# Kernel tuning notes

Measured on AMD Instinct MI355X. Metric: run time of the kernel, lower is better.

The kernel has to match this reference:

```python
import jax, jax.numpy as jnp
import numpy as np

B, C_IN, C_OUT, T, N, KS = 16, 64, 64, 48, 1024, 3

def setup_inputs() -> dict:
    key = jax.random.key(0)
    k1, k2, k3, k4 = jax.random.split(key, 4)
    x = jax.random.normal(k1, (B, C_IN, T, N), dtype=jnp.float32)
    Lk = jax.random.normal(k2, (KS, N, N), dtype=jnp.float32) / np.sqrt(N)
    # kaiming-uniform-like init for theta, uniform for b
    fan_in = C_IN * KS
    bound_t = np.sqrt(6.0 / fan_in)
    theta = jax.random.uniform(k3, (C_IN, C_OUT, KS), dtype=jnp.float32,
                               minval=-bound_t, maxval=bound_t)
    bound_b = 1.0 / np.sqrt(fan_in)
    b = jax.random.uniform(k4, (1, C_OUT, 1, 1), dtype=jnp.float32,
                           minval=-bound_b, maxval=bound_b)
    return {"x": x, "Lk": Lk, "theta": theta, "b": b}

def reference(x, Lk, theta, b):
    # x: [B, c_in, T, N], Lk: [ks, N, N], theta: [c_in, c_out, ks], b: [1, c_out, 1, 1]
    x_c = jnp.einsum('knm,bitm->bitkn', Lk, x)          # [B, c_in, T, ks, N]
    x_gc = jnp.einsum('iok,bitkn->botn', theta, x_c) + b  # [B, c_out, T, N]
    # Align: c_in == c_out -> identity
    return jax.nn.relu(x_gc + x)
```

## Files before the change

kernel.cpp:

```cpp
#include <hip/hip_runtime.h>
#include <hip/hip_bf16.h>
#include <stdint.h>


typedef short bs8 __attribute__((ext_vector_type(8)));
typedef float f32x4 __attribute__((ext_vector_type(4)));

#define NB   16
#define NC   64
#define NT   48
#define NN   1024
#define NKS  3
#define KDIM 3072
#define KT   48

__device__ __forceinline__ short f2bs(float f) {
  uint32_t u = __builtin_bit_cast(uint32_t, f);
  u = (u + 0x7FFFu + ((u >> 16) & 1u)) >> 16;
  return (short)u;
}

__device__ __forceinline__ void gload16(const void* g, void* l) {
  __builtin_amdgcn_global_load_lds(
      (const __attribute__((address_space(1))) void*)g,
      (__attribute__((address_space(3))) void*)l, 16, 0, 0);
}

__global__ __launch_bounds__(256) void k_prep_bt(const float* __restrict__ Lk,
                                                 short* __restrict__ BT) {
  int gid = blockIdx.x * 256 + threadIdx.x;
  int e = gid * 4;
  int k = e >> 20;
  int rem = e & 1048575;
  int n = rem >> 10;
  int m = rem & 1023;
  float4 v = *reinterpret_cast<const float4*>(Lk + e);
  union { short s[4]; uint64_t u; } p;
  p.s[0] = f2bs(v.x); p.s[1] = f2bs(v.y); p.s[2] = f2bs(v.z); p.s[3] = f2bs(v.w);
  *reinterpret_cast<uint64_t*>(BT + (size_t)n * KDIM + k * NN + m) = p.u;
}

__global__ __launch_bounds__(256, 2) void k_step1(const float* __restrict__ x,
                                                  const float* __restrict__ theta,
                                                  short* __restrict__ Y, int b0) {
  __shared__ __align__(16) short th[NKS * 64 * 72];
  __shared__ __align__(16) float xs[64 * 128];
  int tid = threadIdx.x;
  int wave = tid >> 6;
  for (int idx = tid; idx < NC * NC * NKS; idx += 256) {
    int i = idx / (NC * NKS);
    int r = idx - i * (NC * NKS);
    int o = r / NKS;
    int k = r - o * NKS;
    th[(k * 64 + o) * 72 + i] = f2bs(theta[idx]);
  }

  int bid = blockIdx.x;
  int mt  = bid & 7;
  int btl = bid >> 3;
  int b_l = btl / NT;
  int t   = btl - b_l * NT;
  int b   = b0 + b_l;
  const float* xb = x + (size_t)b * (NC * NT * NN) + (size_t)t * NN + mt * 128;

#pragma unroll
  for (int c = 0; c < 8; ++c) {
    int idx = c * 256 + tid;
    int row = idx >> 5, ch = idx & 31;
    gload16(xb + (size_t)row * (NT * NN) + ch * 4,
            xs + (c * 256 + wave * 64) * 4);
  }
  __syncthreads();

  int lane = tid & 63;
  int l15 = lane & 15, lg = lane >> 4;
  size_t yrow0 = (size_t)btl * 64;

  for (int nni = 0; nni < 2; ++nni) {
    int mloc = wave * 32 + nni * 16 + l15;
    float xv[16];
#pragma unroll
    for (int j = 0; j < 16; ++j) {
      int i = ((j >> 3) << 5) + lg * 8 + (j & 7);
      xv[j] = xs[i * 128 + mloc];
    }
    f32x4 acc[3][4];
#pragma unroll
    for (int k = 0; k < 3; ++k)
#pragma unroll
      for (int mi = 0; mi < 4; ++mi)
        acc[k][mi] = (f32x4){0.f, 0.f, 0.f, 0.f};

#pragma unroll
    for (int ks = 0; ks < 2; ++ks) {
      bs8 bfrag;
#pragma unroll
      for (int j = 0; j < 8; ++j) bfrag[j] = f2bs(xv[ks * 8 + j]);
#pragma unroll
      for (int mi = 0; mi < 4; ++mi) {
#pragma unroll
        for (int k = 0; k < 3; ++k) {
          const bs8* ap = reinterpret_cast<const bs8*>(
              &th[(k * 64 + mi * 16 + l15) * 72 + ks * 32 + lg * 8]);
          acc[k][mi] = __builtin_amdgcn_mfma_f32_16x16x32_bf16(
              *ap, bfrag, acc[k][mi], 0, 0, 0);
        }
      }
    }
    int mcol = mt * 128 + mloc;
#pragma unroll
    for (int k = 0; k < 3; ++k)
#pragma unroll
      for (int mi = 0; mi < 4; ++mi)
#pragma unroll
        for (int q = 0; q < 4; ++q) {
          int o = mi * 16 + lg * 4 + q;
          Y[(yrow0 + o) * KDIM + k * NN + mcol] = f2bs(acc[k][mi][q]);
        }
  }
}


__device__ __forceinline__ void stage_tile(const short* __restrict__ src,
                                           short* lds, int tid) {
  int wave = tid >> 6;
#pragma unroll
  for (int c = 0; c < 4; ++c) {
    int idx = c * 256 + tid;
    int row = idx >> 3, c8 = idx & 7;
    int c8s = c8 ^ (row & 7);
    gload16(src + (size_t)row * KDIM + c8s * 8,
            lds + (c * 256 + wave * 64) * 8);
  }
}

#define VMC(N) asm volatile("s_waitcnt vmcnt(" #N ")" ::: "memory")
#define BARR() __builtin_amdgcn_s_barrier();

#define READ_AB(P)                                                        \
  _Pragma("unroll") for (int j = 0; j < 4; ++j)                           \
    _Pragma("unroll") for (int ks = 0; ks < 2; ++ks) {                    \
      int rw = (2 * j + wr) * 16 + l15;                                   \
      af[j][ks] = *(const bs8*)&AL[(P) * 8192 + rw * 64 +                 \
                    ((ks * 32 + lg * 8) ^ ((rw & 7) << 3))];              \
      int rwb = (2 * j + wc) * 16 + l15;                                  \
      bf[j][ks] = *(const bs8*)&BL[(P) * 8192 + rwb * 64 +                \
                    ((ks * 32 + lg * 8) ^ ((rwb & 7) << 3))];             \
    }

#define COMPUTE()                                                           \
  __builtin_amdgcn_s_setprio(1);                                            \
  _Pragma("unroll") for (int ks = 0; ks < 2; ++ks)                          \
    _Pragma("unroll") for (int j = 0; j < 4; ++j)                           \
      _Pragma("unroll") for (int i = 0; i < 4; ++i)                         \
        acc[j][i] = __builtin_amdgcn_mfma_f32_16x16x32_bf16(                \
            af[j][ks], bf[i][ks], acc[j][i], 0, 0, 0);                      \
  __builtin_amdgcn_s_setprio(0);

#define TILE(t, P, S)                                                       \
  {                                                                         \
    bs8 af[4][2], bf[4][2];                                                 \
    if (S) {                                                                \
      stage_tile(Yb + ((t) + 1) * 64, AL + ((P) ^ 1) * 8192, tid);          \
      stage_tile(BTb + ((t) + 1) * 64, BL + ((P) ^ 1) * 8192, tid);         \
    }                                                                       \
    READ_AB(P);                                                             \
    COMPUTE();                                                              \
    if (S) {                                                                \
      VMC(0);                                                               \
      BARR();                                                               \
    }                                                                       \
  }

__global__ __launch_bounds__(256, 2) void k_gemm(const short* __restrict__ Y,
                                                 const short* __restrict__ BT,
                                                 const float* __restrict__ x,
                                                 const float* __restrict__ bias,
                                                 float* __restrict__ out,
                                                 int b0, int nwg) {
  __shared__ __align__(16) short AL[2 * 8192];
  __shared__ __align__(16) short BL[2 * 8192];

  int bid = blockIdx.x;
  int cpx = nwg >> 3;
  int swz = (bid & 7) * cpx + (bid >> 3);
  int colb = swz & 7;
  int rowb = swz >> 3;

  int tid = threadIdx.x;
  int lane = tid & 63, wave = tid >> 6;
  int wr = wave >> 1, wc = wave & 1;
  int l15 = lane & 15, lg = lane >> 4;
  int row0 = rowb * 128, col0 = colb * 128;

  const short* Yb  = Y  + (size_t)row0 * KDIM;
  const short* BTb = BT + (size_t)col0 * KDIM;

  f32x4 acc[4][4];
#pragma unroll
  for (int j = 0; j < 4; ++j)
#pragma unroll
    for (int i = 0; i < 4; ++i) acc[j][i] = (f32x4){0.f, 0.f, 0.f, 0.f};

  stage_tile(Yb,  AL, tid);
  stage_tile(BTb, BL, tid);
  VMC(0);
  BARR();

  for (int t = 0; t < KT - 2; t += 2) {
    TILE(t,     0, 1);
    TILE(t + 1, 1, 1);
  }
  TILE(KT - 2, 0, 1);
  TILE(KT - 1, 1, 0);

#pragma unroll
  for (int j = 0; j < 4; ++j) {
#pragma unroll
    for (int q = 0; q < 4; ++q) {
      int r = row0 + (2 * j + wr) * 16 + lg * 4 + q;
      int o = r & 63;
      int btl = r >> 6;
      int tt = btl % NT;
      int bb = b0 + btl / NT;
      float bo = bias[o];
      size_t obase = ((size_t)(bb * 64 + o) * NT + tt) * NN;
#pragma unroll
      for (int i = 0; i < 4; ++i) {
        int n = col0 + (2 * i + wc) * 16 + l15;
        size_t oidx = obase + n;
        float v = acc[j][i][q] + bo + x[oidx];
        out[oidx] = v > 0.f ? v : 0.f;
      }
    }
  }
}

extern "C" void kernel_launch(void* const* d_in, const int* in_sizes, int n_in,
                              void* d_out, int out_size, void* d_ws, size_t ws_size,
                              hipStream_t stream) {
  const float* x     = (const float*)d_in[0];
  const float* Lk    = (const float*)d_in[1];
  const float* theta = (const float*)d_in[2];
  const float* bias  = (const float*)d_in[3];
  float* out = (float*)d_out;

  char* ws = (char*)d_ws;
  short* BT = (short*)ws;
  short* Y  = (short*)(ws + (size_t)(8u << 20));
  size_t avail = ws_size > ((size_t)8u << 20) ? ws_size - ((size_t)8u << 20) : 0;
  size_t perB = (size_t)NT * NC * KDIM * 2;
  int bc = 16;
  while (bc > 1 && (size_t)bc * perB > avail) bc >>= 1;

  k_prep_bt<<<dim3(3072), dim3(256), 0, stream>>>(Lk, BT);
  for (int b0 = 0; b0 < NB; b0 += bc) {
    k_step1<<<dim3(bc * 384), dim3(256), 0, stream>>>(x, theta, Y, b0);
    int nwg = bc * 192;
    k_gemm<<<dim3(nwg), dim3(256), 0, stream>>>(Y, BT, x, bias, out, b0, nwg);
  }
}
```

Measured before the change: 543.7 us.

## Restructure GEMM to 256x256 tiles with 32x32 MFMA and triple-buffered A

Moves the main GEMM to 256x256 output tiles per 512-thread workgroup and switches from 16x16x32 to 32x32x16 bf16 MFMA. Only the A operand (Y) is staged through LDS, now with a three-slot ring buffer. Each wave reads its B fragments (BT) directly from global memory into registers instead of through LDS. The aim is more reuse per tile, fewer LDS reads per MFMA and better overlap of loads with compute. In exchange it uses more registers and LDS per workgroup, launches fewer workgroups, and the uncached direct global B loads may add latency.

```diff
diff --git a/kernel.cpp b/kernel.cpp
--- a/kernel.cpp
+++ b/kernel.cpp
@@ -5,6 +5,7 @@
 
 typedef short bs8 __attribute__((ext_vector_type(8)));
 typedef float f32x4 __attribute__((ext_vector_type(4)));
+typedef float f32x16 __attribute__((ext_vector_type(16)));
 
 #define NB   16
 #define NC   64
@@ -121,119 +122,119 @@
 }
 
 
-__device__ __forceinline__ void stage_tile(const short* __restrict__ src,
-                                           short* lds, int tid) {
-  int wave = tid >> 6;
+__device__ __forceinline__ void stage_tile32(const short* __restrict__ src,
+                                             short* lds, int tid) {
 #pragma unroll
   for (int c = 0; c < 4; ++c) {
-    int idx = c * 256 + tid;
+    int idx = c * 512 + tid;
     int row = idx >> 3, c8 = idx & 7;
     int c8s = c8 ^ (row & 7);
-    gload16(src + (size_t)row * KDIM + c8s * 8,
-            lds + (c * 256 + wave * 64) * 8);
+    gload16(src + (size_t)row * KDIM + c8s * 8, lds + idx * 8);
   }
 }
 
 #define VMC(N) asm volatile("s_waitcnt vmcnt(" #N ")" ::: "memory")
 #define BARR() __builtin_amdgcn_s_barrier();
 
-#define READ_AB(P)                                                        \
-  _Pragma("unroll") for (int j = 0; j < 4; ++j)                           \
-    _Pragma("unroll") for (int ks = 0; ks < 2; ++ks) {                    \
-      int rw = (2 * j + wr) * 16 + l15;                                   \
-      af[j][ks] = *(const bs8*)&AL[(P) * 8192 + rw * 64 +                 \
-                    ((ks * 32 + lg * 8) ^ ((rw & 7) << 3))];              \
-      int rwb = (2 * j + wc) * 16 + l15;                                  \
-      bf[j][ks] = *(const bs8*)&BL[(P) * 8192 + rwb * 64 +                \
-                    ((ks * 32 + lg * 8) ^ ((rwb & 7) << 3))];             \
-    }
-
-#define COMPUTE()                                                           \
+#define READ_A32(DST, P, AB)                                                \
+  _Pragma("unroll") for (int e = 0; e < 2; ++e)                             \
+    _Pragma("unroll") for (int ks = 0; ks < 4; ++ks) {                      \
+      int rw = (4 * (P) + 2 * e + wr) * 32 + l31;                           \
+      DST[e][ks] = *(const bs8*)&AL[(AB) * 16384 + rw * 64 +                \
+                    (((ks * 2 + hi) ^ (rw & 7)) * 8)];                      \
+    }
+
+#define COMPUTE32(P)                                                        \
   __builtin_amdgcn_s_setprio(1);                                            \
-  _Pragma("unroll") for (int ks = 0; ks < 2; ++ks)                          \
-    _Pragma("unroll") for (int j = 0; j < 4; ++j)                           \
-      _Pragma("unroll") for (int i = 0; i < 4; ++i)                         \
-        acc[j][i] = __builtin_amdgcn_mfma_f32_16x16x32_bf16(                \
-            af[j][ks], bf[i][ks], acc[j][i], 0, 0, 0);                      \
+  _Pragma("unroll") for (int ks = 0; ks < 4; ++ks)                          \
+    _Pragma("unroll") for (int e = 0; e < 2; ++e)                           \
+      _Pragma("unroll") for (int i = 0; i < 2; ++i)                         \
+        acc[2 * (P) + e][i] = __builtin_amdgcn_mfma_f32_32x32x16_bf16(      \
+            af[e][ks], bf[i][ks], acc[2 * (P) + e][i], 0, 0, 0);            \
   __builtin_amdgcn_s_setprio(0);
 
-#define TILE(t, P, S)                                                       \
+#define TILE(t, AB)                                                         \
   {                                                                         \
-    bs8 af[4][2], bf[4][2];                                                 \
-    if (S) {                                                                \
-      stage_tile(Yb + ((t) + 1) * 64, AL + ((P) ^ 1) * 8192, tid);          \
-      stage_tile(BTb + ((t) + 1) * 64, BL + ((P) ^ 1) * 8192, tid);         \
-    }                                                                       \
-    READ_AB(P);                                                             \
-    COMPUTE();                                                              \
-    if (S) {                                                                \
-      VMC(0);                                                               \
-      BARR();                                                               \
-    }                                                                       \
-  }
-
-__global__ __launch_bounds__(256, 2) void k_gemm(const short* __restrict__ Y,
+    bs8 bf[2][4], af[2][4];                                                 \
+    _Pragma("unroll") for (int i = 0; i < 2; ++i)                           \
+      _Pragma("unroll") for (int ks = 0; ks < 4; ++ks)                      \
+        bf[i][ks] = *(const bs8*)(BTf + (size_t)i * (128 * KDIM) +          \
+                                  (t) * 64 + ks * 16);                      \
+    READ_A32(af, 0, AB);                                                    \
+    BARR();                                                                 \
+    if ((t) < KT - 2)                                                       \
+      stage_tile32(Yb + ((t) + 2) * 64, AL + (((AB) + 2) % 3) * 16384, tid);\
+    COMPUTE32(0);                                                           \
+    READ_A32(af, 1, AB);                                                    \
+    BARR();                                                                 \
+    COMPUTE32(1);                                                           \
+  }
+
+__global__ __launch_bounds__(512, 2) void k_gemm(const short* __restrict__ Y,
                                                  const short* __restrict__ BT,
                                                  const float* __restrict__ x,
                                                  const float* __restrict__ bias,
                                                  float* __restrict__ out,
                                                  int b0, int nwg) {
-  __shared__ __align__(16) short AL[2 * 8192];
-  __shared__ __align__(16) short BL[2 * 8192];
+  __shared__ __align__(16) short AL[3 * 16384];
 
   int bid = blockIdx.x;
   int cpx = nwg >> 3;
   int swz = (bid & 7) * cpx + (bid >> 3);
-  int colb = swz & 7;
-  int rowb = swz >> 3;
+  int colb = swz & 3;
+  int rowb = swz >> 2;
 
   int tid = threadIdx.x;
   int lane = tid & 63, wave = tid >> 6;
-  int wr = wave >> 1, wc = wave & 1;
-  int l15 = lane & 15, lg = lane >> 4;
-  int row0 = rowb * 128, col0 = colb * 128;
-
-  const short* Yb  = Y  + (size_t)row0 * KDIM;
-  const short* BTb = BT + (size_t)col0 * KDIM;
-
-  f32x4 acc[4][4];
+  int wr = wave >> 2, wc = wave & 3;
+  int l31 = lane & 31, hi = lane >> 5;
+  int row0 = rowb * 256, col0 = colb * 256;
+
+  const short* Yb  = Y + (size_t)row0 * KDIM;
+  const short* BTf = BT + (size_t)(col0 + wc * 32 + l31) * KDIM + hi * 8;
+
+  f32x16 acc[4][2];
 #pragma unroll
   for (int j = 0; j < 4; ++j)
 #pragma unroll
-    for (int i = 0; i < 4; ++i) acc[j][i] = (f32x4){0.f, 0.f, 0.f, 0.f};
-
-  stage_tile(Yb,  AL, tid);
-  stage_tile(BTb, BL, tid);
-  VMC(0);
+    for (int i = 0; i < 2; ++i)
+#pragma unroll
+      for (int q = 0; q < 16; ++q) acc[j][i][q] = 0.f;
+
+  stage_tile32(Yb,      AL,         tid);
+  stage_tile32(Yb + 64, AL + 16384, tid);
+  VMC(4);
   BARR();
 
-  for (int t = 0; t < KT - 2; t += 2) {
-    TILE(t,     0, 1);
-    TILE(t + 1, 1, 1);
-  }
-  TILE(KT - 2, 0, 1);
-  TILE(KT - 1, 1, 0);
-
-#pragma unroll
-  for (int j = 0; j < 4; ++j) {
-#pragma unroll
-    for (int q = 0; q < 4; ++q) {
-      int r = row0 + (2 * j + wr) * 16 + lg * 4 + q;
-      int o = r & 63;
-      int btl = r >> 6;
-      int tt = btl % NT;
-      int bb = b0 + btl / NT;
-      float bo = bias[o];
-      size_t obase = ((size_t)(bb * 64 + o) * NT + tt) * NN;
-#pragma unroll
-      for (int i = 0; i < 4; ++i) {
-        int n = col0 + (2 * i + wc) * 16 + l15;
-        size_t oidx = obase + n;
-        float v = acc[j][i][q] + bo + x[oidx];
-        out[oidx] = v > 0.f ? v : 0.f;
+  for (int t = 0; t < KT; t += 3) {
+    TILE(t,     0);
+    TILE(t + 1, 1);
+    TILE(t + 2, 2);
+  }
+
+#pragma unroll
+  for (int P = 0; P < 2; ++P)
+#pragma unroll
+    for (int e = 0; e < 2; ++e) {
+      int absf = 4 * P + 2 * e + wr;
+#pragma unroll
+      for (int q = 0; q < 16; ++q) {
+        int r = row0 + absf * 32 + (q & 3) + 8 * (q >> 2) + 4 * hi;
+        int o = r & 63;
+        int btl = r >> 6;
+        int tt = btl % NT;
+        int bb = b0 + btl / NT;
+        float bo = bias[o];
+        size_t obase = ((size_t)(bb * 64 + o) * NT + tt) * NN;
+#pragma unroll
+        for (int i = 0; i < 2; ++i) {
+          int n = col0 + (4 * i + wc) * 32 + l31;
+          size_t oidx = obase + n;
+          float v = acc[2 * P + e][i][q] + bo + x[oidx];
+          out[oidx] = v > 0.f ? v : 0.f;
+        }
       }
     }
-  }
 }
 
 extern "C" void kernel_launch(void* const* d_in, const int* in_sizes, int n_in,
@@ -256,7 +257,7 @@
   k_prep_bt<<<dim3(3072), dim3(256), 0, stream>>>(Lk, BT);
   for (int b0 = 0; b0 < NB; b0 += bc) {
     k_step1<<<dim3(bc * 384), dim3(256), 0, stream>>>(x, theta, Y, b0);
-    int nwg = bc * 192;
-    k_gemm<<<dim3(nwg), dim3(256), 0, stream>>>(Y, BT, x, bias, out, b0, nwg);
-  }
-}
+    int nwg = bc * 48;
+    k_gemm<<<dim3(nwg), dim3(512), 0, stream>>>(Y, BT, x, bias, out, b0, nwg);
+  }
+}
```

After: 681.5 us. 25.3% more time.
